# Performance work log

Measured on AMD Instinct MI355X. Metric: run time of the kernel, lower is better.

## Reference

```python
import jax, jax.numpy as jnp
import numpy as np

GROUP_SIZE = 128  # per-group quantization granularity along infeatures (K)


def setup_inputs() -> dict:
    key = jax.random.key(0)
    k1, k2, k3, k4, k5 = jax.random.split(key, 5)
    B, K, N, G = 32, 4096, 11008, 4096 // GROUP_SIZE
    x = jax.random.normal(k1, (B, K), dtype=jnp.float16)
    # packed int4 weights: 8 nibbles per int32 along K
    qweight = jax.random.randint(k2, (K // 8, N), 0, 2**31 - 1, dtype=jnp.int32)
    # packed int4 zero points: 8 nibbles per int32 along N, one row per group
    qzeros = jax.random.randint(k3, (G, N // 8), 0, 2**31 - 1, dtype=jnp.int32)
    scales = (jax.random.uniform(k4, (G, N), dtype=jnp.float16) * 0.02 + 0.001).astype(jnp.float16)
    bias = (jax.random.normal(k5, (N,), dtype=jnp.float16) * 0.01).astype(jnp.float16)
    return {"x": x, "qweight": qweight, "qzeros": qzeros, "scales": scales, "bias": bias}


def _unpack_int4(packed, axis):
    # packed int32 -> 8 unsigned 4-bit values, expanded along `axis`
    shifts = (jnp.arange(8, dtype=jnp.int32) * 4)
    shape = [1] * (packed.ndim + 1)
    shape[axis + 1] = 8
    vals = (jnp.expand_dims(packed, axis + 1) >> shifts.reshape(shape)) & 0xF
    new_shape = list(packed.shape)
    new_shape[axis] *= 8
    return vals.reshape(new_shape)


def reference(x, qweight, qzeros, scales, bias):
    K = qweight.shape[0] * 8
    N = qweight.shape[1]
    G = scales.shape[0]
    # unpack weights along K: [K, N] int32 in [0, 15]
    q = _unpack_int4(qweight, axis=0)
    # unpack zero points along N: [G, N]
    z = _unpack_int4(qzeros, axis=1)
    # GPTQ dequant: W[k, n] = scales[g(k), n] * (q[k, n] - (z[g(k), n] + 1))
    qg = q.reshape(G, GROUP_SIZE, N)
    W = ((qg - (z + 1)[:, None, :]).astype(jnp.float16) * scales[:, None, :]).reshape(K, N)
    out = jnp.matmul(x, W, preferred_element_type=jnp.float32).astype(jnp.float16)
    return out + bias
```

## Files before the change

kernel.cpp:

```cpp
#include <hip/hip_runtime.h>
#include <hip/hip_bf16.h>


#define M_ROWS 32
#define K_DIM  4096
#define N_DIM  11008
#define GS     128
#define BN     64
#define KSPLIT 8
#define BKR    (K_DIM / KSPLIT)
#define NGRP   (BKR / GS)
#define OUT_ELEMS (M_ROWS * N_DIM)

#define WS_PART_OFF (256 * 1024)

typedef __bf16 bf16x8 __attribute__((ext_vector_type(8)));
typedef float  f32x4  __attribute__((ext_vector_type(4)));

__global__ __launch_bounds__(256)
void pack_x_kernel(const float* __restrict__ x, __bf16* __restrict__ xp) {
    const int gt = blockIdx.x * 256 + threadIdx.x;
    const int c  = gt >> 6;
    const int l  = gt & 63;
    const int t  = c & 1;
    const int b  = c >> 1;
    const int m  = 16 * t + (l & 15);
    const int k0 = 32 * b + (l >> 4) * 8;
    const float4 f0 = *(const float4*)(&x[m * K_DIM + k0]);
    const float4 f1 = *(const float4*)(&x[m * K_DIM + k0 + 4]);
    bf16x8 hv;
    hv[0] = (__bf16)f0.x; hv[1] = (__bf16)f0.y;
    hv[2] = (__bf16)f0.z; hv[3] = (__bf16)f0.w;
    hv[4] = (__bf16)f1.x; hv[5] = (__bf16)f1.y;
    hv[6] = (__bf16)f1.z; hv[7] = (__bf16)f1.w;
    *(bf16x8*)(&xp[(size_t)gt * 8]) = hv;
}

__global__ __launch_bounds__(256, 4)
void gptq_mfma_kernel(const __bf16* __restrict__ xp,
                      const int* __restrict__ qweight,
                      const int* __restrict__ qzeros,
                      const float* __restrict__ scales,
                      float* __restrict__ part)
{
    const int tid  = threadIdx.x;
    const int lane = tid & 63;
    const int wave = tid >> 6;
    const int n0   = blockIdx.x * BN;
    const int kb   = blockIdx.y;

    const int col  = lane & 15;
    const int quad = lane >> 4;
    const int n    = n0 + wave * 16 + col;

    f32x4 acc0 = {0.f, 0.f, 0.f, 0.f};
    f32x4 acc1 = {0.f, 0.f, 0.f, 0.f};

    #pragma unroll
    for (int gl = 0; gl < NGRP; ++gl) {
        const int g  = kb * NGRP + gl;
        const int zw = qzeros[g * (N_DIM / 8) + (n >> 3)];
        const float sc = scales[g * N_DIM + n];
        const float zs = (float)(((zw >> ((n & 7) * 4)) & 0xF) + 1) * sc;

        #pragma unroll
        for (int ks = 0; ks < 4; ++ks) {
            const int wrow = kb * (BKR / 8) + gl * (GS / 8) + ks * 4 + quad;
            const int w    = qweight[wrow * N_DIM + n];
            bf16x8 bfrag;
            #pragma unroll
            for (int j = 0; j < 8; ++j) {
                const float qf = (float)((w >> (4 * j)) & 0xF);
                bfrag[j] = (__bf16)(qf * sc - zs);
            }
            const int b = kb * 16 + gl * 4 + ks;
            const bf16x8 a0 = *(const bf16x8*)(&xp[((b * 2 + 0) * 64 + lane) * 8]);
            const bf16x8 a1 = *(const bf16x8*)(&xp[((b * 2 + 1) * 64 + lane) * 8]);
            acc0 = __builtin_amdgcn_mfma_f32_16x16x32_bf16(a0, bfrag, acc0, 0, 0, 0);
            acc1 = __builtin_amdgcn_mfma_f32_16x16x32_bf16(a1, bfrag, acc1, 0, 0, 0);
        }
    }

    float* p = part + (size_t)kb * OUT_ELEMS;
    #pragma unroll
    for (int r = 0; r < 4; ++r) {
        const int m = quad * 4 + r;
        p[m * N_DIM + n]        = acc0[r];
        p[(16 + m) * N_DIM + n] = acc1[r];
    }
}

__global__ __launch_bounds__(256)
void reduce_kernel(const float* __restrict__ part,
                   const float* __restrict__ bias,
                   float* __restrict__ out)
{
    const int i    = blockIdx.x * 256 + threadIdx.x;
    const int base = i * 4;
    if (base >= OUT_ELEMS) return;
    const int n = base % N_DIM;
    f32x4 s = *(const f32x4*)(&part[base]);
    #pragma unroll
    for (int kb = 1; kb < KSPLIT; ++kb) {
        const f32x4 v = *(const f32x4*)(&part[(size_t)kb * OUT_ELEMS + base]);
        s += v;
    }
    const f32x4 bv = *(const f32x4*)(&bias[n]);
    s += bv;
    *(f32x4*)(&out[base]) = s;
}

extern "C" void kernel_launch(void* const* d_in, const int* in_sizes, int n_in,
                              void* d_out, int out_size, void* d_ws, size_t ws_size,
                              hipStream_t stream) {
    const float* x       = (const float*)d_in[0];
    const int*   qweight = (const int*)d_in[1];
    const int*   qzeros  = (const int*)d_in[2];
    const float* scales  = (const float*)d_in[3];
    const float* bias    = (const float*)d_in[4];
    float*       out     = (float*)d_out;

    __bf16* xp   = (__bf16*)d_ws;
    float*  part = (float*)((char*)d_ws + WS_PART_OFF);

    pack_x_kernel<<<64, 256, 0, stream>>>(x, xp);

    dim3 grid(N_DIM / BN, KSPLIT);
    gptq_mfma_kernel<<<grid, 256, 0, stream>>>(xp, qweight, qzeros, scales, part);

    reduce_kernel<<<(OUT_ELEMS / 4 + 255) / 256, 256, 0, stream>>>(part, bias, out);
}
```

Baseline: 89.19 us.

## Fuse split-K reduction into GEMM kernel via in-block LDS reduction

Moves the split-K decomposition inside each block: a 512-thread block now runs 8 waves, one per K slice, over a 32-column N tile. The waves reduce their partials through padded LDS and add the bias before writing the output. This removes the separate reduce kernel, one launch, and the global round trip of 8 full-size fp32 partial buffers. The grid shrinks to 344 blocks, each with 16 KB+ of LDS, and each wave now does two 16-column fragments, which may reduce occupancy and parallelism on a 256-CU part.

```diff
diff --git a/kernel.cpp b/kernel.cpp
--- a/kernel.cpp
+++ b/kernel.cpp
@@ -6,13 +6,11 @@
 #define K_DIM  4096
 #define N_DIM  11008
 #define GS     128
-#define BN     64
+#define BN     32
 #define KSPLIT 8
 #define BKR    (K_DIM / KSPLIT)
 #define NGRP   (BKR / GS)
-#define OUT_ELEMS (M_ROWS * N_DIM)
-
-#define WS_PART_OFF (256 * 1024)
+#define LDSW   33
 
 typedef __bf16 bf16x8 __attribute__((ext_vector_type(8)));
 typedef float  f32x4  __attribute__((ext_vector_type(4)));
@@ -36,78 +34,82 @@
     *(bf16x8*)(&xp[(size_t)gt * 8]) = hv;
 }
 
-__global__ __launch_bounds__(256, 4)
-void gptq_mfma_kernel(const __bf16* __restrict__ xp,
-                      const int* __restrict__ qweight,
-                      const int* __restrict__ qzeros,
-                      const float* __restrict__ scales,
-                      float* __restrict__ part)
+__global__ __launch_bounds__(512, 4)
+void gptq_fused_kernel(const __bf16* __restrict__ xp,
+                       const int* __restrict__ qweight,
+                       const int* __restrict__ qzeros,
+                       const float* __restrict__ scales,
+                       const float* __restrict__ bias,
+                       float* __restrict__ out)
 {
+    __shared__ float lds[KSPLIT * M_ROWS * LDSW];
+
     const int tid  = threadIdx.x;
     const int lane = tid & 63;
-    const int wave = tid >> 6;
+    const int kb   = tid >> 6;
     const int n0   = blockIdx.x * BN;
-    const int kb   = blockIdx.y;
 
     const int col  = lane & 15;
     const int quad = lane >> 4;
-    const int n    = n0 + wave * 16 + col;
+    const int nA   = n0 + col;
+    const int nB   = n0 + 16 + col;
 
-    f32x4 acc0 = {0.f, 0.f, 0.f, 0.f};
-    f32x4 acc1 = {0.f, 0.f, 0.f, 0.f};
+    f32x4 accA0 = {0.f,0.f,0.f,0.f}, accA1 = {0.f,0.f,0.f,0.f};
+    f32x4 accB0 = {0.f,0.f,0.f,0.f}, accB1 = {0.f,0.f,0.f,0.f};
 
     #pragma unroll
     for (int gl = 0; gl < NGRP; ++gl) {
-        const int g  = kb * NGRP + gl;
-        const int zw = qzeros[g * (N_DIM / 8) + (n >> 3)];
-        const float sc = scales[g * N_DIM + n];
-        const float zs = (float)(((zw >> ((n & 7) * 4)) & 0xF) + 1) * sc;
+        const int g   = kb * NGRP + gl;
+        const int zwA = qzeros[g * (N_DIM / 8) + (nA >> 3)];
+        const int zwB = qzeros[g * (N_DIM / 8) + (nB >> 3)];
+        const float scA = scales[g * N_DIM + nA];
+        const float scB = scales[g * N_DIM + nB];
+        const float zsA = (float)(((zwA >> ((nA & 7) * 4)) & 0xF) + 1) * scA;
+        const float zsB = (float)(((zwB >> ((nB & 7) * 4)) & 0xF) + 1) * scB;
 
         #pragma unroll
         for (int ks = 0; ks < 4; ++ks) {
             const int wrow = kb * (BKR / 8) + gl * (GS / 8) + ks * 4 + quad;
-            const int w    = qweight[wrow * N_DIM + n];
-            bf16x8 bfrag;
+            const int wA = qweight[wrow * N_DIM + nA];
+            const int wB = qweight[wrow * N_DIM + nB];
+            bf16x8 bfA, bfB;
             #pragma unroll
             for (int j = 0; j < 8; ++j) {
-                const float qf = (float)((w >> (4 * j)) & 0xF);
-                bfrag[j] = (__bf16)(qf * sc - zs);
+                bfA[j] = (__bf16)((float)((wA >> (4 * j)) & 0xF) * scA - zsA);
+                bfB[j] = (__bf16)((float)((wB >> (4 * j)) & 0xF) * scB - zsB);
             }
             const int b = kb * 16 + gl * 4 + ks;
             const bf16x8 a0 = *(const bf16x8*)(&xp[((b * 2 + 0) * 64 + lane) * 8]);
             const bf16x8 a1 = *(const bf16x8*)(&xp[((b * 2 + 1) * 64 + lane) * 8]);
-            acc0 = __builtin_amdgcn_mfma_f32_16x16x32_bf16(a0, bfrag, acc0, 0, 0, 0);
-            acc1 = __builtin_amdgcn_mfma_f32_16x16x32_bf16(a1, bfrag, acc1, 0, 0, 0);
+            accA0 = __builtin_amdgcn_mfma_f32_16x16x32_bf16(a0, bfA, accA0, 0, 0, 0);
+            accA1 = __builtin_amdgcn_mfma_f32_16x16x32_bf16(a1, bfA, accA1, 0, 0, 0);
+            accB0 = __builtin_amdgcn_mfma_f32_16x16x32_bf16(a0, bfB, accB0, 0, 0, 0);
+            accB1 = __builtin_amdgcn_mfma_f32_16x16x32_bf16(a1, bfB, accB1, 0, 0, 0);
         }
     }
 
-    float* p = part + (size_t)kb * OUT_ELEMS;
+    float* slab = &lds[kb * M_ROWS * LDSW];
     #pragma unroll
     for (int r = 0; r < 4; ++r) {
         const int m = quad * 4 + r;
-        p[m * N_DIM + n]        = acc0[r];
-        p[(16 + m) * N_DIM + n] = acc1[r];
+        slab[m * LDSW + col]             = accA0[r];
+        slab[(16 + m) * LDSW + col]      = accA1[r];
+        slab[m * LDSW + 16 + col]        = accB0[r];
+        slab[(16 + m) * LDSW + 16 + col] = accB1[r];
     }
-}
+    __syncthreads();
 
-__global__ __launch_bounds__(256)
-void reduce_kernel(const float* __restrict__ part,
-                   const float* __restrict__ bias,
-                   float* __restrict__ out)
-{
-    const int i    = blockIdx.x * 256 + threadIdx.x;
-    const int base = i * 4;
-    if (base >= OUT_ELEMS) return;
-    const int n = base % N_DIM;
-    f32x4 s = *(const f32x4*)(&part[base]);
     #pragma unroll
-    for (int kb = 1; kb < KSPLIT; ++kb) {
-        const f32x4 v = *(const f32x4*)(&part[(size_t)kb * OUT_ELEMS + base]);
-        s += v;
+    for (int i = 0; i < 2; ++i) {
+        const int idx = i * 512 + tid;
+        const int m   = idx >> 5;
+        const int c   = idx & 31;
+        float s = 0.f;
+        #pragma unroll
+        for (int w = 0; w < KSPLIT; ++w)
+            s += lds[w * M_ROWS * LDSW + m * LDSW + c];
+        out[m * N_DIM + n0 + c] = s + bias[n0 + c];
     }
-    const f32x4 bv = *(const f32x4*)(&bias[n]);
-    s += bv;
-    *(f32x4*)(&out[base]) = s;
 }
 
 extern "C" void kernel_launch(void* const* d_in, const int* in_sizes, int n_in,
@@ -120,13 +122,9 @@
     const float* bias    = (const float*)d_in[4];
     float*       out     = (float*)d_out;
 
-    __bf16* xp   = (__bf16*)d_ws;
-    float*  part = (float*)((char*)d_ws + WS_PART_OFF);
+    __bf16* xp = (__bf16*)d_ws;
 
     pack_x_kernel<<<64, 256, 0, stream>>>(x, xp);
-
-    dim3 grid(N_DIM / BN, KSPLIT);
-    gptq_mfma_kernel<<<grid, 256, 0, stream>>>(xp, qweight, qzeros, scales, part);
-
-    reduce_kernel<<<(OUT_ELEMS / 4 + 255) / 256, 256, 0, stream>>>(part, bias, out);
+    gptq_fused_kernel<<<N_DIM / BN, 512, 0, stream>>>(xp, qweight, qzeros,
+                                                      scales, bias, out);
 }
```

Result: no change. 88.02 us (-1.3%).
